# Performance work log

Hardware: AMD Instinct MI355X
Metric: run time of the kernel (lower is better)

Reference implementation:

```python
import jax, jax.numpy as jnp
import numpy as np

IMAGE_SIZE = 128
PATCH_SIZE = 8
BOND_DIM = 128
CP_RANK = 64
EMBED_DIM = 512
BATCH = 512
GRID = IMAGE_SIZE // PATCH_SIZE            # 16
NUM_PATCHES = GRID * GRID                  # 256
DEPTH = 4                                  # log4(256)
LEVEL_NODES = [64, 16, 4, 1]


def setup_inputs() -> dict:
    key = jax.random.key(0)
    ks = jax.random.split(key, 32)
    s = 0.02
    inp = {
        "x": jax.random.normal(ks[0], (BATCH, 1, IMAGE_SIZE, IMAGE_SIZE), jnp.float32),
        "W_patch": jax.random.normal(ks[1], (PATCH_SIZE * PATCH_SIZE, BOND_DIM), jnp.float32) * s,
        "b_patch": jnp.zeros((BOND_DIM,), jnp.float32),
        "pos": jax.random.normal(ks[2], (1, NUM_PATCHES, BOND_DIM), jnp.float32),
        "gamma": jnp.ones((BOND_DIM,), jnp.float32),
        "beta": jnp.zeros((BOND_DIM,), jnp.float32),
        "W_head": jax.random.normal(ks[3], (BOND_DIM, EMBED_DIM), jnp.float32) * s,
        "b_head": jnp.zeros((EMBED_DIM,), jnp.float32),
    }
    for lvl, n in enumerate(LEVEL_NODES):
        # per-node distinct CP factors: 4 children in_dim->rank, then rank->out_dim
        inp[f"f{lvl}"] = jax.random.normal(ks[4 + 2 * lvl], (n, 4, BOND_DIM, CP_RANK), jnp.float32) * s
        inp[f"o{lvl}"] = jax.random.normal(ks[5 + 2 * lvl], (n, CP_RANK, BOND_DIM), jnp.float32) * s
    return inp


def _patchify(x):
    # 'b c (h p1) (w p2) -> b (h w) (p1 p2 c)', c == 1
    b = x.shape[0]
    x = x.reshape(b, 1, GRID, PATCH_SIZE, GRID, PATCH_SIZE)
    x = x.transpose(0, 2, 4, 3, 5, 1)                  # b h w p1 p2 c
    return x.reshape(b, NUM_PATCHES, PATCH_SIZE * PATCH_SIZE)


def _quad_group(x, grid):
    # 'b (h w) c -> b (h/2 w/2) (h2 w2) c' with 2x2 blocks
    b, _, c = x.shape
    g2 = grid // 2
    x = x.reshape(b, g2, 2, g2, 2, c).transpose(0, 1, 3, 2, 4, 5)
    return x.reshape(b, g2 * g2, 4, c)


def _cp_level(x, f, o):
    # x: [b, n, 4, C]; f: [n, 4, C, R]; o: [n, R, C]
    u = jnp.einsum('bnqc,nqcr->bnqr', x, f)
    p = jnp.prod(u, axis=2)                            # [b, n, R]
    return jnp.einsum('bnr,nrc->bnc', p, o)


def reference(x, W_patch, b_patch, pos, f0, o0, f1, o1, f2, o2, f3, o3,
              gamma, beta, W_head, b_head):
    h = _patchify(x) @ W_patch + b_patch               # [b, 256, C]
    h = h + pos
    grid = GRID
    for f, o in ((f0, o0), (f1, o1), (f2, o2), (f3, o3)):
        h = _cp_level(_quad_group(h, grid), f, o)
        grid //= 2
    h = h[:, 0, :]                                     # squeeze node dim
    mu = jnp.mean(h, axis=-1, keepdims=True)
    var = jnp.var(h, axis=-1, keepdims=True)
    h = (h - mu) / jnp.sqrt(var + 1e-5) * gamma + beta
    out = h @ W_head + b_head
    n = jnp.maximum(jnp.linalg.norm(out, axis=-1, keepdims=True), 1e-12)
    return out / n
```

## Files before the change

kernel.cpp:

```cpp
#include <hip/hip_runtime.h>
#include <hip/hip_bf16.h>

#define BATCH     512
#define IMG       128
#define PS        8
#define GRID_P    16
#define NP        256
#define C         128
#define R         64
#define E         512

typedef float f32x4 __attribute__((ext_vector_type(4)));
typedef short s16x8 __attribute__((ext_vector_type(8)));

__device__ __forceinline__ unsigned short f2bf(float x) {
    unsigned int u = __float_as_uint(x);
    u += 0x7fffu + ((u >> 16) & 1u);
    return (unsigned short)(u >> 16);
}


__global__ __launch_bounds__(256) void prep_all_kernel(
    const float* __restrict__ f0, const float* __restrict__ f1,
    const float* __restrict__ f2, const float* __restrict__ f3,
    const float* __restrict__ o0, const float* __restrict__ o1,
    const float* __restrict__ o2, const float* __restrict__ o3,
    const float* __restrict__ Wh, const float* __restrict__ Wp,
    const float* __restrict__ pos, const float* __restrict__ bp,
    unsigned short* __restrict__ fTL, unsigned short* __restrict__ oT,
    unsigned short* __restrict__ WhT, unsigned short* __restrict__ WfT,
    float* __restrict__ pf)
{
    __shared__ float ls[128 * 68];
    __shared__ float red[64 * 4];
    const int bi = blockIdx.x, t = threadIdx.x;

    if (bi < 256) {
        const float* src = f0 + (size_t)bi * 8192;
#pragma unroll
        for (int i = 0; i < 8; ++i) {
            const int fi = (t + 256 * i) * 4;
            const int c = fi >> 6, r = fi & 63;
            *(float4*)(ls + c * 68 + r) = *(const float4*)(src + fi);
        }
        __syncthreads();

        const int w = t >> 6, lane = t & 63;
        const int m = lane & 15, g = lane >> 4;

        f32x4 acc[4];
#pragma unroll
        for (int nt = 0; nt < 4; ++nt) acc[nt] = (f32x4){0.f, 0.f, 0.f, 0.f};
#pragma unroll
        for (int kt = 0; kt < 4; ++kt) {
            s16x8 afr;
#pragma unroll
            for (int e = 0; e < 8; ++e)
                afr[e] = (short)f2bf(ls[(kt * 32 + g * 8 + e) * 68 + w * 16 + m]);
#pragma unroll
            for (int nt = 0; nt < 4; ++nt) {
                const float* wr = Wp + (size_t)(nt * 16 + m) * 128 + kt * 32 + g * 8;
                const float4 b0 = *(const float4*)wr;
                const float4 b1 = *(const float4*)(wr + 4);
                s16x8 bfr;
                bfr[0] = (short)f2bf(b0.x); bfr[1] = (short)f2bf(b0.y);
                bfr[2] = (short)f2bf(b0.z); bfr[3] = (short)f2bf(b0.w);
                bfr[4] = (short)f2bf(b1.x); bfr[5] = (short)f2bf(b1.y);
                bfr[6] = (short)f2bf(b1.z); bfr[7] = (short)f2bf(b1.w);
                acc[nt] = __builtin_amdgcn_mfma_f32_16x16x32_bf16(afr, bfr, acc[nt], 0, 0, 0);
            }
        }
        unsigned short* D = WfT + (size_t)bi * 4096;
#pragma unroll
        for (int nt = 0; nt < 4; ++nt)
#pragma unroll
            for (int j = 0; j < 4; ++j) {
                const int Q = nt * 16 + m;
                const int N = (((Q >> 5) * 4 + w) * 64 + ((Q >> 3) & 3) * 16 + (g * 4 + j)) * 8 + (Q & 7);
                D[N] = f2bf(acc[nt][j]);
            }

        {
            const int r = t & 63, half = t >> 6;
            const int n0 = bi >> 2, q = bi & 3;
            const int pp = (2 * (n0 >> 3) + (q >> 1)) * GRID_P + 2 * (n0 & 7) + (q & 1);
            const float* posr = pos + (size_t)pp * C;
            float s = 0.f;
#pragma unroll 8
            for (int e = 0; e < 32; ++e) {
                const int c = half * 32 + e;
                s += (posr[c] + bp[c]) * ls[c * 68 + r];
            }
            red[r * 4 + half] = s;
        }
        __syncthreads();
        if (t < 64)
            pf[bi * 64 + t] = red[t * 4 + 0] + red[t * 4 + 1] + red[t * 4 + 2] + red[t * 4 + 3];
    } else if (bi < 340) {
        const int ti = bi - 256;
        const float* src;
        if      (ti < 64) src = f1 + (size_t)ti * 8192;
        else if (ti < 80) src = f2 + (size_t)(ti - 64) * 8192;
        else              src = f3 + (size_t)(ti - 80) * 8192;
        unsigned short* dst = fTL + (size_t)ti * 8192;
#pragma unroll
        for (int i = 0; i < 8; ++i) {
            const int fi = (t + 256 * i) * 4;
            const int c = fi >> 6, r = fi & 63;
            *(float4*)(ls + c * 68 + r) = *(const float4*)(src + fi);
        }
        __syncthreads();
        if (ti < 64) {
#pragma unroll
            for (int k = 0; k < 4; ++k) {
                const int unit = t + 256 * k;
                const int grp = unit >> 6, lp = unit & 63;
                const int kt = grp >> 2, nt = grp & 3;
                const int mp = lp & 15, gp = lp >> 4;
                s16x8 v;
#pragma unroll
                for (int e = 0; e < 8; ++e)
                    v[e] = (short)f2bf(ls[(kt * 32 + gp * 8 + e) * 68 + nt * 16 + mp]);
                *(s16x8*)(dst + (size_t)(grp * 64 + lp) * 8) = v;
            }
        } else {
            const int rr = t >> 2, seg = t & 3;
            unsigned int* d32 = (unsigned int*)(dst + rr * 128 + seg * 32);
#pragma unroll
            for (int ii = 0; ii < 16; ++ii) {
                const int c = seg * 32 + ii * 2;
                const unsigned int lo = f2bf(ls[c * 68 + rr]);
                const unsigned int hi = f2bf(ls[(c + 1) * 68 + rr]);
                d32[ii] = lo | (hi << 16);
            }
        }
    } else if (bi < 425) {
        const int oi = bi - 340;
        const float* src;
        if      (oi < 64) src = o0 + (size_t)oi * 8192;
        else if (oi < 80) src = o1 + (size_t)(oi - 64) * 8192;
        else if (oi < 84) src = o2 + (size_t)(oi - 80) * 8192;
        else              src = o3 + (size_t)(oi - 84) * 8192;
        unsigned short* dst = oT + (size_t)oi * 8192;
#pragma unroll
        for (int i = 0; i < 8; ++i) {
            const int fi = (t + 256 * i) * 4;
            const int r = fi >> 7, c = fi & 127;
            *(float4*)(ls + r * 132 + c) = *(const float4*)(src + fi);
        }
        __syncthreads();
        if (oi < 80) {
#pragma unroll
            for (int k = 0; k < 4; ++k) {
                const int unit = t + 256 * k;
                const int grp = unit >> 6, lp = unit & 63;
                const int ct = grp >> 1, kt = grp & 1;
                const int mp = lp & 15, gp = lp >> 4;
                s16x8 v;
#pragma unroll
                for (int e = 0; e < 8; ++e)
                    v[e] = (short)f2bf(ls[(kt * 32 + gp * 8 + e) * 132 + ct * 16 + mp]);
                *(s16x8*)(dst + (size_t)(grp * 64 + lp) * 8) = v;
            }
        } else {
            const int cc = t >> 1, seg = t & 1;
            unsigned int* d32 = (unsigned int*)(dst + cc * 64 + seg * 32);
#pragma unroll
            for (int ii = 0; ii < 16; ++ii) {
                const int r = seg * 32 + ii * 2;
                const unsigned int lo = f2bf(ls[r * 132 + cc]);
                const unsigned int hi = f2bf(ls[(r + 1) * 132 + cc]);
                d32[ii] = lo | (hi << 16);
            }
        }
    } else {
        const int j = bi - 425;
#pragma unroll
        for (int i = 0; i < 8; ++i) {
            const int fi = (t + 256 * i) * 4;
            const int c = fi >> 6, e = fi & 63;
            *(float4*)(ls + c * 68 + e) = *(const float4*)(Wh + (size_t)c * E + j * 64 + e);
        }
        __syncthreads();
        const int rr = t >> 2, seg = t & 3;
        unsigned int* d32 = (unsigned int*)(WhT + (size_t)(j * 64 + rr) * 128 + seg * 32);
#pragma unroll
        for (int ii = 0; ii < 16; ++ii) {
            const int c = seg * 32 + ii * 2;
            const unsigned int lo = f2bf(ls[c * 68 + rr]);
            const unsigned int hi = f2bf(ls[(c + 1) * 68 + rr]);
            d32[ii] = lo | (hi << 16);
        }
    }
}

__global__ __launch_bounds__(256, 3) void level01_fused(
    const float* __restrict__ x,
    const unsigned short* __restrict__ WfT,
    const float* __restrict__ pf,
    const unsigned short* __restrict__ oT,
    const unsigned short* __restrict__ fT1,
    unsigned short* __restrict__ h2)
{
    __shared__ __align__(16) float          us1[4 * 16 * 68];
    __shared__ __align__(16) unsigned short ps0[4 * 16 * 72];
    __shared__ __align__(16) unsigned short ps1[16 * 72];
    __shared__ __align__(16) unsigned short h1s[4 * 16 * 136];

    const int bi = blockIdx.x;
    const int n1 = ((bi & 7) << 1) | ((bi >> 3) & 1);
    const int btile = bi >> 4;
    const int t = threadIdx.x, w = t >> 6, lane = t & 63;
    const int m = lane & 15, g = lane >> 4;
    const int bt = btile * 16;

    const int y1g = n1 >> 2, x1g = n1 & 3;
    const int Ry0 = y1g * 32, Rx0 = x1g * 32;
    const int n0 = (2 * y1g + (w >> 1)) * 8 + 2 * x1g + (w & 1);

    s16x8 a[4][2];
    {
        const int rbase = 16 * (w >> 1);
        const int cbase = 16 * (w & 1);
        const float* xb = x + (size_t)(bt + m) * (IMG * IMG);
#pragma unroll
        for (int q = 0; q < 4; ++q) {
            const int rq = rbase + 8 * (q >> 1) + g;
            const int cc = cbase + 8 * (q & 1);
#pragma unroll
            for (int kt = 0; kt < 2; ++kt) {
                const float* px = xb + (size_t)(Ry0 + rq + kt * 4) * IMG + Rx0 + cc;
                const float4 p0 = *(const float4*)px;
                const float4 p1 = *(const float4*)(px + 4);
                s16x8 fr;
                fr[0] = (short)f2bf(p0.x); fr[1] = (short)f2bf(p0.y);
                fr[2] = (short)f2bf(p0.z); fr[3] = (short)f2bf(p0.w);
                fr[4] = (short)f2bf(p1.x); fr[5] = (short)f2bf(p1.y);
                fr[6] = (short)f2bf(p1.z); fr[7] = (short)f2bf(p1.w);
                a[q][kt] = fr;
            }
        }
    }

    f32x4 accu[4][4];
#pragma unroll
    for (int q = 0; q < 4; ++q) {
        const float* pfq = pf + (size_t)(n0 * 4 + q) * 64;
#pragma unroll
        for (int nt = 0; nt < 4; ++nt) {
            const float pv = pfq[nt * 16 + m];
            accu[q][nt] = (f32x4){pv, pv, pv, pv};
        }
    }
#pragma unroll
    for (int q = 0; q < 4; ++q) {
        const unsigned short* Wq = WfT + (size_t)(n0 * 4 + q) * 4096;
#pragma unroll
        for (int kt = 0; kt < 2; ++kt) {
#pragma unroll
            for (int nt = 0; nt < 4; ++nt) {
                const s16x8 bfr = *(const s16x8*)(Wq + (size_t)((kt * 4 + nt) * 64 + lane) * 8);
                accu[q][nt] = __builtin_amdgcn_mfma_f32_16x16x32_bf16(a[q][kt], bfr, accu[q][nt], 0, 0, 0);
            }
        }
    }

    unsigned short* myps = ps0 + w * (16 * 72);
#pragma unroll
    for (int nt = 0; nt < 4; ++nt) {
        const f32x4 pr = accu[0][nt] * accu[1][nt] * accu[2][nt] * accu[3][nt];
#pragma unroll
        for (int j = 0; j < 4; ++j)
            myps[(g * 4 + j) * 72 + nt * 16 + m] = f2bf(pr[j]);
    }

    {
        s16x8 ap[2];
#pragma unroll
        for (int kt = 0; kt < 2; ++kt)
            ap[kt] = *(const s16x8*)(myps + m * 72 + kt * 32 + g * 8);
        const unsigned short* oTn = oT + (size_t)n0 * 8192;
        unsigned short* myh = h1s + w * (16 * 136);
#pragma unroll
        for (int ct = 0; ct < 8; ++ct) {
            f32x4 aco = (f32x4){0.f, 0.f, 0.f, 0.f};
#pragma unroll
            for (int kt = 0; kt < 2; ++kt) {
                const s16x8 bfr = *(const s16x8*)(oTn + (size_t)((ct * 2 + kt) * 64 + lane) * 8);
                aco = __builtin_amdgcn_mfma_f32_16x16x32_bf16(ap[kt], bfr, aco, 0, 0, 0);
            }
#pragma unroll
            for (int j = 0; j < 4; ++j)
                myh[(g * 4 + j) * 136 + ct * 16 + m] = f2bf(aco[j]);
        }
    }

    {
        const unsigned short* myh = h1s + w * (16 * 136);
        const unsigned short* fq = fT1 + (size_t)(n1 * 4 + w) * 8192;
        f32x4 au[4];
#pragma unroll
        for (int nt = 0; nt < 4; ++nt) au[nt] = (f32x4){0.f, 0.f, 0.f, 0.f};
#pragma unroll
        for (int kt = 0; kt < 4; ++kt) {
            const int koff = kt * 32 + g * 8;
            const s16x8 afr = *(const s16x8*)(myh + m * 136 + koff);
#pragma unroll
            for (int nt = 0; nt < 4; ++nt) {
                const s16x8 bfr = *(const s16x8*)(fq + (size_t)((kt * 4 + nt) * 64 + lane) * 8);
                au[nt] = __builtin_amdgcn_mfma_f32_16x16x32_bf16(afr, bfr, au[nt], 0, 0, 0);
            }
        }
#pragma unroll
        for (int nt = 0; nt < 4; ++nt)
#pragma unroll
            for (int j = 0; j < 4; ++j)
                us1[(w * 16 + g * 4 + j) * 68 + nt * 16 + m] = au[nt][j];
    }
    __syncthreads();

    {
        const int pb = t >> 4, r0 = (t & 15) * 4;
        const f32x4 u0 = *(const f32x4*)(us1 + (0 * 16 + pb) * 68 + r0);
        const f32x4 u1 = *(const f32x4*)(us1 + (1 * 16 + pb) * 68 + r0);
        const f32x4 u2 = *(const f32x4*)(us1 + (2 * 16 + pb) * 68 + r0);
        const f32x4 u3 = *(const f32x4*)(us1 + (3 * 16 + pb) * 68 + r0);
        const f32x4 p = u0 * u1 * u2 * u3;
        uint2 v;
        v.x = (unsigned int)f2bf(p[0]) | ((unsigned int)f2bf(p[1]) << 16);
        v.y = (unsigned int)f2bf(p[2]) | ((unsigned int)f2bf(p[3]) << 16);
        *(uint2*)(ps1 + pb * 72 + r0) = v;
    }
    __syncthreads();

    {
        s16x8 ap[2];
#pragma unroll
        for (int kt = 0; kt < 2; ++kt)
            ap[kt] = *(const s16x8*)(ps1 + m * 72 + kt * 32 + g * 8);
        const unsigned short* oTn = oT + (size_t)(64 + n1) * 8192;
#pragma unroll
        for (int i = 0; i < 2; ++i) {
            const int ct = w * 2 + i;
            f32x4 aco = (f32x4){0.f, 0.f, 0.f, 0.f};
#pragma unroll
            for (int kt = 0; kt < 2; ++kt) {
                const s16x8 bfr = *(const s16x8*)(oTn + (size_t)((ct * 2 + kt) * 64 + lane) * 8);
                aco = __builtin_amdgcn_mfma_f32_16x16x32_bf16(ap[kt], bfr, aco, 0, 0, 0);
            }
#pragma unroll
            for (int j = 0; j < 4; ++j)
                h2[((size_t)(bt + g * 4 + j) * 16 + n1) * C + ct * 16 + m] = f2bf(aco[j]);
        }
    }
}

__global__ __launch_bounds__(256, 1) void tail_kernel(
    const unsigned short* __restrict__ h2,
    const unsigned short* __restrict__ fT2,
    const unsigned short* __restrict__ oT2,
    const unsigned short* __restrict__ fT3,
    const unsigned short* __restrict__ oT3,
    const float* __restrict__ gamma, const float* __restrict__ beta,
    const unsigned short* __restrict__ WhT,
    const float* __restrict__ bh,
    float* __restrict__ out)
{
    __shared__ __align__(16) float          us3[4 * 16 * 68];
    __shared__ __align__(16) unsigned short ps2[4 * 16 * 72];
    __shared__ __align__(16) unsigned short ps3[16 * 72];
    __shared__ __align__(16) unsigned short h3s[16 * 4 * 136];
    __shared__ __align__(16) float          h4s[16 * 132];
    __shared__ __align__(16) unsigned short hns[16 * 136];
    __shared__ float red[16 * 4];

    const int bt = blockIdx.x * 16;
    const int t = threadIdx.x, w = t >> 6, lane = t & 63;
    const int m = lane & 15, g = lane >> 4;

    {
        const int n2 = w;
        const int y1 = n2 >> 1, x1 = n2 & 1;

        s16x8 xa[4][4];
#pragma unroll
        for (int q = 0; q < 4; ++q) {
            const int pidx = (2 * y1 + (q >> 1)) * 4 + 2 * x1 + (q & 1);
            const unsigned short* xq = h2 + ((size_t)(bt + m) * 16 + pidx) * C;
#pragma unroll
            for (int kt = 0; kt < 4; ++kt)
                xa[q][kt] = *(const s16x8*)(xq + kt * 32 + g * 8);
        }

        f32x4 acc_u[4][4];
#pragma unroll
        for (int q = 0; q < 4; ++q)
#pragma unroll
            for (int nt = 0; nt < 4; ++nt) acc_u[q][nt] = (f32x4){0.f, 0.f, 0.f, 0.f};
#pragma unroll
        for (int q = 0; q < 4; ++q) {
            const unsigned short* fq = fT2 + (size_t)(n2 * 4 + q) * R * C;
#pragma unroll
            for (int kt = 0; kt < 4; ++kt) {
                const int koff = kt * 32 + g * 8;
#pragma unroll
                for (int nt = 0; nt < 4; ++nt) {
                    const s16x8 bfr = *(const s16x8*)(fq + (size_t)(nt * 16 + m) * C + koff);
                    acc_u[q][nt] = __builtin_amdgcn_mfma_f32_16x16x32_bf16(xa[q][kt], bfr, acc_u[q][nt], 0, 0, 0);
                }
            }
        }

        s16x8 ob[8][2];
        {
            const unsigned short* oTn = oT2 + (size_t)n2 * C * R;
#pragma unroll
            for (int ct = 0; ct < 8; ++ct)
#pragma unroll
                for (int kt = 0; kt < 2; ++kt)
                    ob[ct][kt] = *(const s16x8*)(oTn + (size_t)(ct * 16 + m) * R + kt * 32 + g * 8);
        }

        unsigned short* myps2 = ps2 + w * 16 * 72;
#pragma unroll
        for (int nt = 0; nt < 4; ++nt) {
            const f32x4 p = acc_u[0][nt] * acc_u[1][nt] * acc_u[2][nt] * acc_u[3][nt];
#pragma unroll
            for (int j = 0; j < 4; ++j)
                myps2[(g * 4 + j) * 72 + nt * 16 + m] = f2bf(p[j]);
        }
        f32x4 aco[8];
#pragma unroll
        for (int ct = 0; ct < 8; ++ct) aco[ct] = (f32x4){0.f, 0.f, 0.f, 0.f};
#pragma unroll
        for (int kt = 0; kt < 2; ++kt) {
            const int koff = kt * 32 + g * 8;
            const s16x8 av = *(const s16x8*)(myps2 + m * 72 + koff);
#pragma unroll
            for (int ct = 0; ct < 8; ++ct)
                aco[ct] = __builtin_amdgcn_mfma_f32_16x16x32_bf16(av, ob[ct][kt], aco[ct], 0, 0, 0);
        }
#pragma unroll
        for (int ct = 0; ct < 8; ++ct)
#pragma unroll
            for (int j = 0; j < 4; ++j)
                h3s[((g * 4 + j) * 4 + n2) * 136 + ct * 16 + m] = f2bf(aco[ct][j]);
    }
    __syncthreads();

    {
        const int q = w;
        s16x8 fb[4][4];
        {
            const unsigned short* fq = fT3 + (size_t)q * R * C;
#pragma unroll
            for (int kt = 0; kt < 4; ++kt)
#pragma unroll
                for (int nt = 0; nt < 4; ++nt)
                    fb[kt][nt] = *(const s16x8*)(fq + (size_t)(nt * 16 + m) * C + kt * 32 + g * 8);
        }
        f32x4 acc_u[4];
#pragma unroll
        for (int nt = 0; nt < 4; ++nt) acc_u[nt] = (f32x4){0.f, 0.f, 0.f, 0.f};
#pragma unroll
        for (int kt = 0; kt < 4; ++kt) {
            const int koff = kt * 32 + g * 8;
            const s16x8 av = *(const s16x8*)(h3s + (m * 4 + q) * 136 + koff);
#pragma unroll
            for (int nt = 0; nt < 4; ++nt)
                acc_u[nt] = __builtin_amdgcn_mfma_f32_16x16x32_bf16(av, fb[kt][nt], acc_u[nt], 0, 0, 0);
        }
#pragma unroll
        for (int nt = 0; nt < 4; ++nt)
#pragma unroll
            for (int j = 0; j < 4; ++j)
                us3[(q * 16 + g * 4 + j) * 68 + nt * 16 + m] = acc_u[nt][j];
    }
    __syncthreads();
    {
        const int pb = t >> 4, r0 = (t & 15) * 4;
        const f32x4 u0 = *(const f32x4*)(us3 + (0 * 16 + pb) * 68 + r0);
        const f32x4 u1 = *(const f32x4*)(us3 + (1 * 16 + pb) * 68 + r0);
        const f32x4 u2 = *(const f32x4*)(us3 + (2 * 16 + pb) * 68 + r0);
        const f32x4 u3 = *(const f32x4*)(us3 + (3 * 16 + pb) * 68 + r0);
        const f32x4 p = u0 * u1 * u2 * u3;
        uint2 v;
        v.x = (unsigned int)f2bf(p[0]) | ((unsigned int)f2bf(p[1]) << 16);
        v.y = (unsigned int)f2bf(p[2]) | ((unsigned int)f2bf(p[3]) << 16);
        *(uint2*)(ps3 + pb * 72 + r0) = v;
    }
    __syncthreads();
    {
        s16x8 ap[2];
#pragma unroll
        for (int kt = 0; kt < 2; ++kt)
            ap[kt] = *(const s16x8*)(ps3 + m * 72 + kt * 32 + g * 8);
#pragma unroll
        for (int i = 0; i < 2; ++i) {
            f32x4 aco = (f32x4){0.f, 0.f, 0.f, 0.f};
            const int ct = w * 2 + i;
#pragma unroll
            for (int kt = 0; kt < 2; ++kt) {
                const s16x8 bfr = *(const s16x8*)(oT3 + (size_t)(ct * 16 + m) * R + kt * 32 + g * 8);
                aco = __builtin_amdgcn_mfma_f32_16x16x32_bf16(ap[kt], bfr, aco, 0, 0, 0);
            }
#pragma unroll
            for (int j = 0; j < 4; ++j)
                h4s[(g * 4 + j) * 132 + ct * 16 + m] = aco[j];
        }
    }
    __syncthreads();

    {
        const int rb = w * 4 + g;
        const int c0 = m * 8;
        const f32x4 v0 = *(const f32x4*)(h4s + rb * 132 + c0);
        const f32x4 v1 = *(const f32x4*)(h4s + rb * 132 + c0 + 4);
        float s  = v0[0] + v0[1] + v0[2] + v0[3] + v1[0] + v1[1] + v1[2] + v1[3];
        float ss = v0[0]*v0[0] + v0[1]*v0[1] + v0[2]*v0[2] + v0[3]*v0[3]
                 + v1[0]*v1[0] + v1[1]*v1[1] + v1[2]*v1[2] + v1[3]*v1[3];
#pragma unroll
        for (int off = 1; off < 16; off <<= 1) {
            s  += __shfl_xor(s, off);
            ss += __shfl_xor(ss, off);
        }
        const float mu   = s * (1.f / C);
        const float var  = ss * (1.f / C) - mu * mu;
        const float rstd = rsqrtf(var + 1e-5f);
        const f32x4 ga0 = *(const f32x4*)(gamma + c0);
        const f32x4 ga1 = *(const f32x4*)(gamma + c0 + 4);
        const f32x4 be0 = *(const f32x4*)(beta + c0);
        const f32x4 be1 = *(const f32x4*)(beta + c0 + 4);
        unsigned int o32[4];
        float hv[8];
#pragma unroll
        for (int k = 0; k < 4; ++k) hv[k]     = (v0[k] - mu) * rstd * ga0[k] + be0[k];
#pragma unroll
        for (int k = 0; k < 4; ++k) hv[4 + k] = (v1[k] - mu) * rstd * ga1[k] + be1[k];
#pragma unroll
        for (int k = 0; k < 4; ++k)
            o32[k] = (unsigned int)f2bf(hv[2*k]) | ((unsigned int)f2bf(hv[2*k+1]) << 16);
        *(uint4*)(hns + rb * 136 + c0) = *(uint4*)o32;
    }
    __syncthreads();

    {
        f32x4 acc[8];
#pragma unroll
        for (int nt = 0; nt < 8; ++nt) {
            const int e = w * 128 + nt * 16 + m;
            const float bv = bh[e];
            acc[nt] = (f32x4){bv, bv, bv, bv};
        }
#pragma unroll
        for (int kt = 0; kt < 4; ++kt) {
            const int koff = kt * 32 + g * 8;
            const s16x8 av = *(const s16x8*)(hns + m * 136 + koff);
#pragma unroll
            for (int nt = 0; nt < 8; ++nt) {
                const int e = w * 128 + nt * 16 + m;
                const s16x8 bfr = *(const s16x8*)(WhT + (size_t)e * 128 + koff);
                acc[nt] = __builtin_amdgcn_mfma_f32_16x16x32_bf16(av, bfr, acc[nt], 0, 0, 0);
            }
        }
        float sq[4];
#pragma unroll
        for (int j = 0; j < 4; ++j) {
            float s = 0.f;
#pragma unroll
            for (int nt = 0; nt < 8; ++nt) s += acc[nt][j] * acc[nt][j];
#pragma unroll
            for (int off = 1; off < 16; off <<= 1) s += __shfl_xor(s, off);
            sq[j] = s;
        }
        if (m == 0) {
#pragma unroll
            for (int j = 0; j < 4; ++j) red[(g * 4 + j) * 4 + w] = sq[j];
        }
        __syncthreads();
#pragma unroll
        for (int j = 0; j < 4; ++j) {
            const int row = g * 4 + j;
            const float tot = red[row * 4 + 0] + red[row * 4 + 1]
                            + red[row * 4 + 2] + red[row * 4 + 3];
            const float inv = 1.f / fmaxf(sqrtf(tot), 1e-12f);
#pragma unroll
            for (int nt = 0; nt < 8; ++nt) {
                const int e = w * 128 + nt * 16 + m;
                out[(size_t)(bt + row) * E + e] = acc[nt][j] * inv;
            }
        }
    }
}

extern "C" void kernel_launch(void* const* d_in, const int* in_sizes, int n_in,
                              void* d_out, int out_size, void* d_ws, size_t ws_size,
                              hipStream_t stream) {
    const float* x     = (const float*)d_in[0];
    const float* Wp    = (const float*)d_in[1];
    const float* bp    = (const float*)d_in[2];
    const float* pos   = (const float*)d_in[3];
    const float* gamma = (const float*)d_in[4];
    const float* beta  = (const float*)d_in[5];
    const float* Wh    = (const float*)d_in[6];
    const float* bh    = (const float*)d_in[7];
    const float* f0    = (const float*)d_in[8];
    const float* o0    = (const float*)d_in[9];
    const float* f1    = (const float*)d_in[10];
    const float* o1    = (const float*)d_in[11];
    const float* f2    = (const float*)d_in[12];
    const float* o2    = (const float*)d_in[13];
    const float* f3    = (const float*)d_in[14];
    const float* o3    = (const float*)d_in[15];
    float* out = (float*)d_out;

    unsigned short* h2  = (unsigned short*)d_ws;
    unsigned short* fTL = h2 + (size_t)1048576;
    unsigned short* oT  = fTL + (size_t)688128;
    unsigned short* WfT = oT + (size_t)696320;
    unsigned short* WhT = WfT + (size_t)1048576;
    float*          pff = (float*)(WhT + 65536);

    unsigned short* fT1 = fTL;
    unsigned short* fT2 = fTL + (size_t)64 * 8192;
    unsigned short* fT3 = fTL + (size_t)80 * 8192;
    unsigned short* oT2 = oT + (size_t)80 * 8192;
    unsigned short* oT3 = oT + (size_t)84 * 8192;

    prep_all_kernel<<<433, 256, 0, stream>>>(f0, f1, f2, f3, o0, o1, o2, o3,
                                             Wh, Wp, pos, bp,
                                             fTL, oT, WhT, WfT, pff);

    level01_fused<<<16 * 32, 256, 0, stream>>>(x, WfT, pff, oT, fT1, h2);

    tail_kernel<<<32, 256, 0, stream>>>(h2, fT2, oT2, fT3, oT3,
                                        gamma, beta, WhT, bh, out);
}
```

Baseline: 145.4 us.

## Pre-swizzle all weights to MFMA fragment order and stage pixels via LDS

All level-2/3 factor, output and head weights are now written by the prep kernel in per-lane MFMA fragment order, so each wave's B-operand loads become contiguous 16-byte reads instead of strided row gathers. Level01 first loads the 32x32 pixel tile for the batch tile into shared memory with coalesced float4 reads, converting to bf16 once, then builds A fragments from LDS. The intermediate h2 layout is changed to node-major so level-2 reads are contiguous per node. The added LDS buffer (~32KB) forces occupancy down from 3 to 2 blocks per CU, which may reduce latency hiding.

```diff
diff --git a/kernel.cpp b/kernel.cpp
--- a/kernel.cpp
+++ b/kernel.cpp
@@ -110,29 +110,17 @@
             *(float4*)(ls + c * 68 + r) = *(const float4*)(src + fi);
         }
         __syncthreads();
-        if (ti < 64) {
-#pragma unroll
-            for (int k = 0; k < 4; ++k) {
-                const int unit = t + 256 * k;
-                const int grp = unit >> 6, lp = unit & 63;
-                const int kt = grp >> 2, nt = grp & 3;
-                const int mp = lp & 15, gp = lp >> 4;
-                s16x8 v;
-#pragma unroll
-                for (int e = 0; e < 8; ++e)
-                    v[e] = (short)f2bf(ls[(kt * 32 + gp * 8 + e) * 68 + nt * 16 + mp]);
-                *(s16x8*)(dst + (size_t)(grp * 64 + lp) * 8) = v;
-            }
-        } else {
-            const int rr = t >> 2, seg = t & 3;
-            unsigned int* d32 = (unsigned int*)(dst + rr * 128 + seg * 32);
-#pragma unroll
-            for (int ii = 0; ii < 16; ++ii) {
-                const int c = seg * 32 + ii * 2;
-                const unsigned int lo = f2bf(ls[c * 68 + rr]);
-                const unsigned int hi = f2bf(ls[(c + 1) * 68 + rr]);
-                d32[ii] = lo | (hi << 16);
-            }
+#pragma unroll
+        for (int k = 0; k < 4; ++k) {
+            const int unit = t + 256 * k;
+            const int grp = unit >> 6, lp = unit & 63;
+            const int kt = grp >> 2, nt = grp & 3;
+            const int mp = lp & 15, gp = lp >> 4;
+            s16x8 v;
+#pragma unroll
+            for (int e = 0; e < 8; ++e)
+                v[e] = (short)f2bf(ls[(kt * 32 + gp * 8 + e) * 68 + nt * 16 + mp]);
+            *(s16x8*)(dst + (size_t)(grp * 64 + lp) * 8) = v;
         }
     } else if (bi < 425) {
         const int oi = bi - 340;
@@ -149,29 +137,17 @@
             *(float4*)(ls + r * 132 + c) = *(const float4*)(src + fi);
         }
         __syncthreads();
-        if (oi < 80) {
-#pragma unroll
-            for (int k = 0; k < 4; ++k) {
-                const int unit = t + 256 * k;
-                const int grp = unit >> 6, lp = unit & 63;
-                const int ct = grp >> 1, kt = grp & 1;
-                const int mp = lp & 15, gp = lp >> 4;
-                s16x8 v;
-#pragma unroll
-                for (int e = 0; e < 8; ++e)
-                    v[e] = (short)f2bf(ls[(kt * 32 + gp * 8 + e) * 132 + ct * 16 + mp]);
-                *(s16x8*)(dst + (size_t)(grp * 64 + lp) * 8) = v;
-            }
-        } else {
-            const int cc = t >> 1, seg = t & 1;
-            unsigned int* d32 = (unsigned int*)(dst + cc * 64 + seg * 32);
-#pragma unroll
-            for (int ii = 0; ii < 16; ++ii) {
-                const int r = seg * 32 + ii * 2;
-                const unsigned int lo = f2bf(ls[r * 132 + cc]);
-                const unsigned int hi = f2bf(ls[(r + 1) * 132 + cc]);
-                d32[ii] = lo | (hi << 16);
-            }
+#pragma unroll
+        for (int k = 0; k < 4; ++k) {
+            const int unit = t + 256 * k;
+            const int grp = unit >> 6, lp = unit & 63;
+            const int ct = grp >> 1, kt = grp & 1;
+            const int mp = lp & 15, gp = lp >> 4;
+            s16x8 v;
+#pragma unroll
+            for (int e = 0; e < 8; ++e)
+                v[e] = (short)f2bf(ls[(kt * 32 + gp * 8 + e) * 132 + ct * 16 + mp]);
+            *(s16x8*)(dst + (size_t)(grp * 64 + lp) * 8) = v;
         }
     } else {
         const int j = bi - 425;
@@ -182,19 +158,24 @@
             *(float4*)(ls + c * 68 + e) = *(const float4*)(Wh + (size_t)c * E + j * 64 + e);
         }
         __syncthreads();
-        const int rr = t >> 2, seg = t & 3;
-        unsigned int* d32 = (unsigned int*)(WhT + (size_t)(j * 64 + rr) * 128 + seg * 32);
-#pragma unroll
-        for (int ii = 0; ii < 16; ++ii) {
-            const int c = seg * 32 + ii * 2;
-            const unsigned int lo = f2bf(ls[c * 68 + rr]);
-            const unsigned int hi = f2bf(ls[(c + 1) * 68 + rr]);
-            d32[ii] = lo | (hi << 16);
+#pragma unroll
+        for (int k = 0; k < 4; ++k) {
+            const int unit = t + 256 * k;
+            const int gl = unit >> 6, lp = unit & 63;
+            const int kt = gl >> 2, nt_lo = gl & 3;
+            const int mp = lp & 15, gp = lp >> 4;
+            s16x8 v;
+#pragma unroll
+            for (int e = 0; e < 8; ++e)
+                v[e] = (short)f2bf(ls[(kt * 32 + gp * 8 + e) * 68 + nt_lo * 16 + mp]);
+            const int wq = j >> 1;
+            const int nt = (j & 1) * 4 + nt_lo;
+            *(s16x8*)(WhT + (size_t)((wq * 32 + kt * 8 + nt) * 64 + lp) * 8) = v;
         }
     }
 }
 
-__global__ __launch_bounds__(256, 3) void level01_fused(
+__global__ __launch_bounds__(256, 2) void level01_fused(
     const float* __restrict__ x,
     const unsigned short* __restrict__ WfT,
     const float* __restrict__ pf,
@@ -202,6 +183,7 @@
     const unsigned short* __restrict__ fT1,
     unsigned short* __restrict__ h2)
 {
+    __shared__ __align__(16) unsigned short pixs[16 * 1026];
     __shared__ __align__(16) float          us1[4 * 16 * 68];
     __shared__ __align__(16) unsigned short ps0[4 * 16 * 72];
     __shared__ __align__(16) unsigned short ps1[16 * 72];
@@ -218,27 +200,29 @@
     const int Ry0 = y1g * 32, Rx0 = x1g * 32;
     const int n0 = (2 * y1g + (w >> 1)) * 8 + 2 * x1g + (w & 1);
 
+#pragma unroll
+    for (int i = 0; i < 16; ++i) {
+        const int idx = i * 256 + t;
+        const int c4 = idx & 7, rowg = (idx >> 3) & 31, bl = idx >> 8;
+        const float4 p4 = *(const float4*)(x + ((size_t)(bt + bl) * IMG + Ry0 + rowg) * IMG + Rx0 + c4 * 4);
+        uint2 v;
+        v.x = (unsigned int)f2bf(p4.x) | ((unsigned int)f2bf(p4.y) << 16);
+        v.y = (unsigned int)f2bf(p4.z) | ((unsigned int)f2bf(p4.w) << 16);
+        *(uint2*)(pixs + bl * 1026 + rowg * 32 + c4 * 4) = v;
+    }
+    __syncthreads();
+
     s16x8 a[4][2];
     {
         const int rbase = 16 * (w >> 1);
         const int cbase = 16 * (w & 1);
-        const float* xb = x + (size_t)(bt + m) * (IMG * IMG);
 #pragma unroll
         for (int q = 0; q < 4; ++q) {
             const int rq = rbase + 8 * (q >> 1) + g;
             const int cc = cbase + 8 * (q & 1);
 #pragma unroll
-            for (int kt = 0; kt < 2; ++kt) {
-                const float* px = xb + (size_t)(Ry0 + rq + kt * 4) * IMG + Rx0 + cc;
-                const float4 p0 = *(const float4*)px;
-                const float4 p1 = *(const float4*)(px + 4);
-                s16x8 fr;
-                fr[0] = (short)f2bf(p0.x); fr[1] = (short)f2bf(p0.y);
-                fr[2] = (short)f2bf(p0.z); fr[3] = (short)f2bf(p0.w);
-                fr[4] = (short)f2bf(p1.x); fr[5] = (short)f2bf(p1.y);
-                fr[6] = (short)f2bf(p1.z); fr[7] = (short)f2bf(p1.w);
-                a[q][kt] = fr;
-            }
+            for (int kt = 0; kt < 2; ++kt)
+                a[q][kt] = *(const s16x8*)(pixs + m * 1026 + (rq + kt * 4) * 32 + cc);
         }
     }
 
@@ -350,7 +334,7 @@
             }
 #pragma unroll
             for (int j = 0; j < 4; ++j)
-                h2[((size_t)(bt + g * 4 + j) * 16 + n1) * C + ct * 16 + m] = f2bf(aco[j]);
+                h2[((size_t)n1 * BATCH + (bt + g * 4 + j)) * C + ct * 16 + m] = f2bf(aco[j]);
         }
     }
 }
@@ -386,7 +370,7 @@
 #pragma unroll
         for (int q = 0; q < 4; ++q) {
             const int pidx = (2 * y1 + (q >> 1)) * 4 + 2 * x1 + (q & 1);
-            const unsigned short* xq = h2 + ((size_t)(bt + m) * 16 + pidx) * C;
+            const unsigned short* xq = h2 + ((size_t)pidx * BATCH + bt + m) * C;
 #pragma unroll
             for (int kt = 0; kt < 4; ++kt)
                 xa[q][kt] = *(const s16x8*)(xq + kt * 32 + g * 8);
@@ -399,13 +383,12 @@
             for (int nt = 0; nt < 4; ++nt) acc_u[q][nt] = (f32x4){0.f, 0.f, 0.f, 0.f};
 #pragma unroll
         for (int q = 0; q < 4; ++q) {
-            const unsigned short* fq = fT2 + (size_t)(n2 * 4 + q) * R * C;
+            const unsigned short* fq = fT2 + (size_t)(n2 * 4 + q) * 8192;
 #pragma unroll
             for (int kt = 0; kt < 4; ++kt) {
-                const int koff = kt * 32 + g * 8;
 #pragma unroll
                 for (int nt = 0; nt < 4; ++nt) {
-                    const s16x8 bfr = *(const s16x8*)(fq + (size_t)(nt * 16 + m) * C + koff);
+                    const s16x8 bfr = *(const s16x8*)(fq + (size_t)((kt * 4 + nt) * 64 + lane) * 8);
                     acc_u[q][nt] = __builtin_amdgcn_mfma_f32_16x16x32_bf16(xa[q][kt], bfr, acc_u[q][nt], 0, 0, 0);
                 }
             }
@@ -413,12 +396,12 @@
 
         s16x8 ob[8][2];
         {
-            const unsigned short* oTn = oT2 + (size_t)n2 * C * R;
+            const unsigned short* oTn = oT2 + (size_t)n2 * 8192;
 #pragma unroll
             for (int ct = 0; ct < 8; ++ct)
 #pragma unroll
                 for (int kt = 0; kt < 2; ++kt)
-                    ob[ct][kt] = *(const s16x8*)(oTn + (size_t)(ct * 16 + m) * R + kt * 32 + g * 8);
+                    ob[ct][kt] = *(const s16x8*)(oTn + (size_t)((ct * 2 + kt) * 64 + lane) * 8);
         }
 
         unsigned short* myps2 = ps2 + w * 16 * 72;
@@ -452,12 +435,12 @@
         const int q = w;
         s16x8 fb[4][4];
         {
-            const unsigned short* fq = fT3 + (size_t)q * R * C;
+            const unsigned short* fq = fT3 + (size_t)q * 8192;
 #pragma unroll
             for (int kt = 0; kt < 4; ++kt)
 #pragma unroll
                 for (int nt = 0; nt < 4; ++nt)
-                    fb[kt][nt] = *(const s16x8*)(fq + (size_t)(nt * 16 + m) * C + kt * 32 + g * 8);
+                    fb[kt][nt] = *(const s16x8*)(fq + (size_t)((kt * 4 + nt) * 64 + lane) * 8);
         }
         f32x4 acc_u[4];
 #pragma unroll
@@ -501,7 +484,7 @@
             const int ct = w * 2 + i;
 #pragma unroll
             for (int kt = 0; kt < 2; ++kt) {
-                const s16x8 bfr = *(const s16x8*)(oT3 + (size_t)(ct * 16 + m) * R + kt * 32 + g * 8);
+                const s16x8 bfr = *(const s16x8*)(oT3 + (size_t)((ct * 2 + kt) * 64 + lane) * 8);
                 aco = __builtin_amdgcn_mfma_f32_16x16x32_bf16(ap[kt], bfr, aco, 0, 0, 0);
             }
 #pragma unroll
@@ -558,8 +541,7 @@
             const s16x8 av = *(const s16x8*)(hns + m * 136 + koff);
 #pragma unroll
             for (int nt = 0; nt < 8; ++nt) {
-                const int e = w * 128 + nt * 16 + m;
-                const s16x8 bfr = *(const s16x8*)(WhT + (size_t)e * 128 + koff);
+                const s16x8 bfr = *(const s16x8*)(WhT + (size_t)((w * 32 + kt * 8 + nt) * 64 + lane) * 8);
                 acc[nt] = __builtin_amdgcn_mfma_f32_16x16x32_bf16(av, bfr, acc[nt], 0, 0, 0);
             }
         }
```

Result: faster. 134.6 us, median of 2 (-7.4%).
